# Performance work log

Hardware: AMD Instinct MI355X
Metric: run time of the kernel (lower is better)

## Reference

```python
import jax, jax.numpy as jnp
import numpy as np

EMBED_DIM = 1024
NUM_HEADS = 16
HEAD_DIM = EMBED_DIM // NUM_HEADS
SCALE = HEAD_DIM ** -0.5


def setup_inputs() -> dict:
    key = jax.random.key(0)
    k_x, k_wqkv, k_bqkv, k_wp, k_bp = jax.random.split(key, 5)
    B, N = 2, 2048
    x = jax.random.normal(k_x, (B, N, EMBED_DIM), dtype=jnp.float32)
    # torch.nn.Linear default init: U(-1/sqrt(fan_in), 1/sqrt(fan_in))
    lim = 1.0 / np.sqrt(EMBED_DIM)
    W_qkv = jax.random.uniform(k_wqkv, (EMBED_DIM, 3 * EMBED_DIM), jnp.float32, -lim, lim)
    b_qkv = jax.random.uniform(k_bqkv, (3 * EMBED_DIM,), jnp.float32, -lim, lim)
    W_proj = jax.random.uniform(k_wp, (EMBED_DIM, EMBED_DIM), jnp.float32, -lim, lim)
    b_proj = jax.random.uniform(k_bp, (EMBED_DIM,), jnp.float32, -lim, lim)
    return {"x": x, "W_qkv": W_qkv, "b_qkv": b_qkv, "W_proj": W_proj, "b_proj": b_proj}


def reference(x, W_qkv, b_qkv, W_proj, b_proj):
    B, N, C = x.shape
    qkv = x @ W_qkv + b_qkv                              # [B, N, 3C]
    qkv = qkv.reshape(B, N, 3, NUM_HEADS, HEAD_DIM)
    qkv = jnp.transpose(qkv, (2, 0, 3, 1, 4))            # [3, B, H, N, D]
    q, k, v = qkv[0], qkv[1], qkv[2]
    attn = jnp.einsum('bhnd,bhmd->bhnm', q, k) * SCALE   # [B, H, N, N]
    attn = jax.nn.softmax(attn, axis=-1)
    out = jnp.einsum('bhnm,bhmd->bhnd', attn, v)         # [B, H, N, D]
    out = jnp.transpose(out, (0, 2, 1, 3)).reshape(B, N, C)
    return out @ W_proj + b_proj
```

## Files before the change

kernel.cpp:

```cpp
#include <hip/hip_runtime.h>
#include <math.h>

typedef unsigned short u16;
typedef _Float16 f16;
typedef f16 f16x8 __attribute__((ext_vector_type(8)));
typedef __fp16 hp16x2 __attribute__((ext_vector_type(2)));
typedef float f32x4 __attribute__((ext_vector_type(4)));
typedef float f32x16 __attribute__((ext_vector_type(16)));

#define SEQ   2048
#define NH    16
#define HD    64
#define EMB   1024
#define NQKV  3072
#define BATCH 2
#define PSTR  72
#define QSCALE 0.18033688f

__device__ __forceinline__ u16 f2h(float f) {
  union { f16 h; u16 u; } w; w.h = (f16)f; return w.u;
}

__device__ __forceinline__ void gload16(const void* g, void* l) {
  __builtin_amdgcn_global_load_lds(
      (const __attribute__((address_space(1))) unsigned int*)g,
      (__attribute__((address_space(3))) unsigned int*)l, 16, 0, 0);
}

__global__ __launch_bounds__(256) void cvt_x(const float* __restrict__ X,
                                             u16* __restrict__ Xh) {
  const size_t i = ((size_t)blockIdx.x * 256 + threadIdx.x) * 8;
  float4 a = *reinterpret_cast<const float4*>(&X[i]);
  float4 b = *reinterpret_cast<const float4*>(&X[i + 4]);
  union { hp16x2 h2[4]; float4 f; } pk;
  pk.h2[0] = __builtin_amdgcn_cvt_pkrtz(a.x, a.y);
  pk.h2[1] = __builtin_amdgcn_cvt_pkrtz(a.z, a.w);
  pk.h2[2] = __builtin_amdgcn_cvt_pkrtz(b.x, b.y);
  pk.h2[3] = __builtin_amdgcn_cvt_pkrtz(b.z, b.w);
  *reinterpret_cast<float4*>(&Xh[i]) = pk.f;
}

__global__ __launch_bounds__(256) void cvt_wt(const float* __restrict__ W,
                                              u16* __restrict__ Wt,
                                              int K, int N) {
  __shared__ u16 T[64][68];
  const int n0 = blockIdx.x << 6, k0 = blockIdx.y << 6;
  const int t = threadIdx.x;
  const int rr = t >> 4, cc = (t & 15) << 2;
#pragma unroll
  for (int p = 0; p < 4; p++) {
    const int kr = p * 16 + rr;
    float4 v = *reinterpret_cast<const float4*>(&W[(size_t)(k0 + kr) * N + n0 + cc]);
    T[cc + 0][kr] = f2h(v.x); T[cc + 1][kr] = f2h(v.y);
    T[cc + 2][kr] = f2h(v.z); T[cc + 3][kr] = f2h(v.w);
  }
  __syncthreads();
#pragma unroll
  for (int p = 0; p < 4; p++) {
    const int nr = p * 16 + rr;
    union { u16 s[4]; unsigned long long d; } o;
    o.s[0] = T[nr][cc + 0]; o.s[1] = T[nr][cc + 1];
    o.s[2] = T[nr][cc + 2]; o.s[3] = T[nr][cc + 3];
    *reinterpret_cast<unsigned long long*>(&Wt[(size_t)(n0 + nr) * K + k0 + cc]) = o.d;
  }
}

__device__ __forceinline__ void gemm_core(const u16* __restrict__ Ag,
                                          const u16* __restrict__ Bg,
                                          int m0, int n0, int t,
                                          f32x4 acc[4][4]) {
  __shared__ __align__(16) u16 As[128 * 32];
  __shared__ __align__(16) u16 Bs[128 * 32];
  const int lane = t & 63, w = t >> 6;
  const int l15  = lane & 15, quad = lane >> 4;
  const int wm = w >> 1, wn = w & 1;
  const int srow  = lane >> 2;
  const int gslot = (lane & 3) ^ ((srow >> 1) & 3);
  const int xk    = (quad ^ ((l15 >> 1) & 3)) << 3;

  for (int k0 = 0; k0 < EMB; k0 += 32) {
    __syncthreads();
#pragma unroll
    for (int i = 0; i < 2; i++) {
      const int ca = w * 2 + i;
      const int arow = ca * 16 + srow;
      gload16(Ag + (size_t)(m0 + arow) * EMB + k0 + gslot * 8, &As[ca * 512]);
      gload16(Bg + (size_t)(n0 + arow) * EMB + k0 + gslot * 8, &Bs[ca * 512]);
    }
    __syncthreads();
    f16x8 af[4], bf[4];
#pragma unroll
    for (int s = 0; s < 4; s++)
      af[s] = *reinterpret_cast<const f16x8*>(&As[(wm * 64 + s * 16 + l15) * 32 + xk]);
#pragma unroll
    for (int s = 0; s < 4; s++)
      bf[s] = *reinterpret_cast<const f16x8*>(&Bs[(wn * 64 + s * 16 + l15) * 32 + xk]);
#pragma unroll
    for (int i = 0; i < 4; i++)
#pragma unroll
      for (int j = 0; j < 4; j++)
        acc[i][j] = __builtin_amdgcn_mfma_f32_16x16x32_f16(af[i], bf[j], acc[i][j], 0, 0, 0);
  }
}

__global__ __launch_bounds__(256) void k_qkv(const u16* __restrict__ Ag,
                                             const u16* __restrict__ Bg,
                                             const float* __restrict__ bias,
                                             u16* __restrict__ qo,
                                             u16* __restrict__ ko,
                                             u16* __restrict__ vo) {
  const int t = threadIdx.x;
  const int lane = t & 63, w = t >> 6;
  const int l15 = lane & 15, quad = lane >> 4;
  const int wm = w >> 1, wn = w & 1;
  const int m0 = blockIdx.y << 7, n0 = blockIdx.x << 7;
  f32x4 acc[4][4];
#pragma unroll
  for (int i = 0; i < 4; i++)
#pragma unroll
    for (int j = 0; j < 4; j++) acc[i][j] = (f32x4){0.f, 0.f, 0.f, 0.f};
  gemm_core(Ag, Bg, m0, n0, t, acc);
#pragma unroll
  for (int j = 0; j < 4; j++) {
    const int c = n0 + wn * 64 + j * 16 + l15;
    const int which = c >> 10, h = (c >> 6) & 15, d = c & 63;
    const float bv = bias[c];
    const float sc = (which == 0) ? QSCALE : 1.0f;
#pragma unroll
    for (int i = 0; i < 4; i++) {
#pragma unroll
      for (int r = 0; r < 4; r++) {
        const int m  = m0 + wm * 64 + i * 16 + quad * 4 + r;
        const int bb = m >> 11, n = m & (SEQ - 1);
        const u16 val = f2h((acc[i][j][r] + bv) * sc);
        if (which == 2)
          vo[(((size_t)bb * NH + h) * HD + d) * SEQ + n] = val;
        else if (which == 1)
          ko[((((size_t)bb * NH + h) * SEQ) + n) * HD + d] = val;
        else
          qo[((((size_t)bb * NH + h) * SEQ) + n) * HD + d] = val;
      }
    }
  }
}

__global__ __launch_bounds__(256) void k_proj(const u16* __restrict__ Ag,
                                              const u16* __restrict__ Bg,
                                              const float* __restrict__ bias,
                                              float* __restrict__ out) {
  const int t = threadIdx.x;
  const int lane = t & 63, w = t >> 6;
  const int l15 = lane & 15, quad = lane >> 4;
  const int wm = w >> 1, wn = w & 1;
  const int m0 = blockIdx.y << 7, n0 = blockIdx.x << 7;
  f32x4 acc[4][4];
#pragma unroll
  for (int i = 0; i < 4; i++)
#pragma unroll
    for (int j = 0; j < 4; j++) acc[i][j] = (f32x4){0.f, 0.f, 0.f, 0.f};
  gemm_core(Ag, Bg, m0, n0, t, acc);
#pragma unroll
  for (int j = 0; j < 4; j++) {
    const int c = n0 + wn * 64 + j * 16 + l15;
    const float bv = bias[c];
#pragma unroll
    for (int i = 0; i < 4; i++) {
#pragma unroll
      for (int r = 0; r < 4; r++) {
        const int m = m0 + wm * 64 + i * 16 + quad * 4 + r;
        out[(size_t)m * EMB + c] = acc[i][j][r] + bv;
      }
    }
  }
}

__global__ __launch_bounds__(256) void k_attn(const u16* __restrict__ Qg,
                                              const u16* __restrict__ Kg,
                                              const u16* __restrict__ Vtg,
                                              u16* __restrict__ AO) {
  __shared__ __align__(16) u16 Ks[64 * 64];
  __shared__ __align__(16) u16 Vs[64 * 64];
  __shared__ __align__(16) u16 Ps[4 * 32 * PSTR];
  const int t    = threadIdx.x;
  const int lane = t & 63, w = t >> 6;
  const int l31  = lane & 31, hi = lane >> 5;
  const int bh   = blockIdx.y;
  const int q0   = blockIdx.x << 7;
  const size_t base = (size_t)bh * SEQ * HD;

  f16x8 qf[4];
  {
    const u16* qp = Qg + base + (size_t)(q0 + 32 * w + l31) * HD + hi * 8;
#pragma unroll
    for (int c = 0; c < 4; c++) {
      union { float4 f; f16x8 v; } fu;
      fu.f = *reinterpret_cast<const float4*>(qp + c * 16);
      qf[c] = fu.v;
    }
  }

  f32x16 O0 = {}, O1 = {};
  float lsum = 0.f;
  const int fsw = (l31 >> 1) & 7;
  const int srw = lane >> 3, ssl = lane & 7;
  u16* Pw = &Ps[w * 32 * PSTR];

  for (int kt = 0; kt < SEQ; kt += 64) {
    __syncthreads();
#pragma unroll
    for (int i = 0; i < 2; i++) {
      const int ca  = w * 2 + i;
      const int row = ca * 8 + srw;
      const int sg  = (ssl ^ ((row >> 1) & 7)) << 3;
      gload16(Kg  + base + (size_t)(kt + row) * HD + sg, &Ks[ca * 512]);
      gload16(Vtg + base + (size_t)row * SEQ + kt + sg,  &Vs[ca * 512]);
    }
    __syncthreads();

#pragma unroll
    for (int sk = 0; sk < 2; sk++) {
      f32x16 c = {};
#pragma unroll
      for (int cc = 0; cc < 4; cc++) {
        f16x8 kf = *reinterpret_cast<const f16x8*>(
            &Ks[(sk * 32 + l31) * 64 + (((cc * 2 + hi) ^ fsw) << 3)]);
        c = __builtin_amdgcn_mfma_f32_32x32x16_f16(kf, qf[cc], c, 0, 0, 0);
      }
#pragma unroll
      for (int g = 0; g < 4; g++) {
        const float p0 = exp2f(c[4 * g + 0]);
        const float p1 = exp2f(c[4 * g + 1]);
        const float p2 = exp2f(c[4 * g + 2]);
        const float p3 = exp2f(c[4 * g + 3]);
        lsum += (p0 + p1) + (p2 + p3);
        union { hp16x2 h2[2]; unsigned long long d; } pk;
        pk.h2[0] = __builtin_amdgcn_cvt_pkrtz(p0, p1);
        pk.h2[1] = __builtin_amdgcn_cvt_pkrtz(p2, p3);
        *reinterpret_cast<unsigned long long*>(
            &Pw[l31 * PSTR + sk * 32 + g * 8 + 4 * hi]) = pk.d;
      }
    }

#pragma unroll
    for (int cc = 0; cc < 4; cc++) {
      f16x8 pf = *reinterpret_cast<const f16x8*>(&Pw[l31 * PSTR + cc * 16 + hi * 8]);
      f16x8 vf0 = *reinterpret_cast<const f16x8*>(
          &Vs[l31 * 64 + (((cc * 2 + hi) ^ fsw) << 3)]);
      f16x8 vf1 = *reinterpret_cast<const f16x8*>(
          &Vs[(32 + l31) * 64 + (((cc * 2 + hi) ^ fsw) << 3)]);
      O0 = __builtin_amdgcn_mfma_f32_32x32x16_f16(pf, vf0, O0, 0, 0, 0);
      O1 = __builtin_amdgcn_mfma_f32_32x32x16_f16(pf, vf1, O1, 0, 0, 0);
    }
  }

  lsum += __shfl_xor(lsum, 32);
  const int b = bh >> 4, h = bh & 15;
#pragma unroll
  for (int g = 0; g < 4; g++) {
#pragma unroll
    for (int rr = 0; rr < 4; rr++) {
      const int r = g * 4 + rr;
      const int qrow = rr + 8 * g + 4 * hi;
      const float inv = 1.f / __shfl(lsum, qrow, 64);
      const int n = q0 + 32 * w + qrow;
      u16* dst = AO + ((size_t)(b * SEQ + n)) * EMB + h * HD;
      dst[l31]      = f2h(O0[r] * inv);
      dst[32 + l31] = f2h(O1[r] * inv);
    }
  }
}

extern "C" void kernel_launch(void* const* d_in, const int* in_sizes, int n_in,
                              void* d_out, int out_size, void* d_ws, size_t ws_size,
                              hipStream_t stream) {
  (void)in_sizes; (void)n_in; (void)out_size; (void)ws_size;
  const float* x     = (const float*)d_in[0];
  const float* Wqkv  = (const float*)d_in[1];
  const float* bqkv  = (const float*)d_in[2];
  const float* Wproj = (const float*)d_in[3];
  const float* bproj = (const float*)d_in[4];
  float* out = (float*)d_out;

  const size_t NE = (size_t)BATCH * SEQ * EMB;
  u16* q    = (u16*)d_ws;
  u16* k    = q + NE;
  u16* vt   = k + NE;
  u16* aoxh = vt + NE;
  u16* Wt   = aoxh + NE;
  u16* Wpt  = Wt + (size_t)NQKV * EMB;

  cvt_x<<<NE / 2048, 256, 0, stream>>>(x, aoxh);
  dim3 gw1(NQKV / 64, EMB / 64);
  cvt_wt<<<gw1, 256, 0, stream>>>(Wqkv, Wt, EMB, NQKV);
  dim3 gw2(EMB / 64, EMB / 64);
  cvt_wt<<<gw2, 256, 0, stream>>>(Wproj, Wpt, EMB, EMB);

  dim3 gq(NQKV / 128, (BATCH * SEQ) / 128);
  k_qkv<<<gq, 256, 0, stream>>>(aoxh, Wt, bqkv, q, k, vt);

  dim3 ga(SEQ / 128, BATCH * NH);
  k_attn<<<ga, 256, 0, stream>>>(q, k, vt, aoxh);

  dim3 gp(EMB / 128, (BATCH * SEQ) / 128);
  k_proj<<<gp, 256, 0, stream>>>(aoxh, Wpt, bproj, out);
}
```

Measured before the change: 220.7 us.

## Split attention key range across two wave groups and pass P through registers

The attention block grows to 512 threads. Two groups of four waves each cover half of the key sequence for the same 128 query rows, then merge partial O and row sums through shared memory. The P tile no longer goes through an LDS staging buffer: packed fp16 probabilities are rearranged with cross-half shuffles into the MFMA operand layout. This aims to double parallelism per query tile, since the grid is only 512 blocks, and to cut LDS traffic, at the cost of a final reduction step and larger blocks.

```diff
diff --git a/kernel.cpp b/kernel.cpp
--- a/kernel.cpp
+++ b/kernel.cpp
@@ -14,7 +14,6 @@
 #define EMB   1024
 #define NQKV  3072
 #define BATCH 2
-#define PSTR  72
 #define QSCALE 0.18033688f
 
 __device__ __forceinline__ u16 f2h(float f) {
@@ -174,23 +173,26 @@
   }
 }
 
-__global__ __launch_bounds__(256) void k_attn(const u16* __restrict__ Qg,
-                                              const u16* __restrict__ Kg,
-                                              const u16* __restrict__ Vtg,
-                                              u16* __restrict__ AO) {
-  __shared__ __align__(16) u16 Ks[64 * 64];
-  __shared__ __align__(16) u16 Vs[64 * 64];
-  __shared__ __align__(16) u16 Ps[4 * 32 * PSTR];
+__global__ __launch_bounds__(512, 4) void k_attn(const u16* __restrict__ Qg,
+                                                 const u16* __restrict__ Kg,
+                                                 const u16* __restrict__ Vtg,
+                                                 u16* __restrict__ AO) {
+  __shared__ __align__(16) u16 KV[2][2][64 * 64];
+  __shared__ float Lx[256];
   const int t    = threadIdx.x;
   const int lane = t & 63, w = t >> 6;
+  const int grp  = w >> 2, wl = w & 3;
   const int l31  = lane & 31, hi = lane >> 5;
   const int bh   = blockIdx.y;
   const int q0   = blockIdx.x << 7;
   const size_t base = (size_t)bh * SEQ * HD;
 
+  u16* Ks = KV[grp][0];
+  u16* Vs = KV[grp][1];
+
   f16x8 qf[4];
   {
-    const u16* qp = Qg + base + (size_t)(q0 + 32 * w + l31) * HD + hi * 8;
+    const u16* qp = Qg + base + (size_t)(q0 + 32 * wl + l31) * HD + hi * 8;
 #pragma unroll
     for (int c = 0; c < 4; c++) {
       union { float4 f; f16x8 v; } fu;
@@ -203,13 +205,13 @@
   float lsum = 0.f;
   const int fsw = (l31 >> 1) & 7;
   const int srw = lane >> 3, ssl = lane & 7;
-  u16* Pw = &Ps[w * 32 * PSTR];
-
-  for (int kt = 0; kt < SEQ; kt += 64) {
+  const int kbeg = grp << 10;
+
+  for (int kt = kbeg; kt < kbeg + (SEQ / 2); kt += 64) {
     __syncthreads();
 #pragma unroll
     for (int i = 0; i < 2; i++) {
-      const int ca  = w * 2 + i;
+      const int ca  = wl * 2 + i;
       const int row = ca * 8 + srw;
       const int sg  = (ssl ^ ((row >> 1) & 7)) << 3;
       gload16(Kg  + base + (size_t)(kt + row) * HD + sg, &Ks[ca * 512]);
@@ -226,6 +228,7 @@
             &Ks[(sk * 32 + l31) * 64 + (((cc * 2 + hi) ^ fsw) << 3)]);
         c = __builtin_amdgcn_mfma_f32_32x32x16_f16(kf, qf[cc], c, 0, 0, 0);
       }
+      unsigned pw[4][2];
 #pragma unroll
       for (int g = 0; g < 4; g++) {
         const float p0 = exp2f(c[4 * g + 0]);
@@ -233,39 +236,73 @@
         const float p2 = exp2f(c[4 * g + 2]);
         const float p3 = exp2f(c[4 * g + 3]);
         lsum += (p0 + p1) + (p2 + p3);
-        union { hp16x2 h2[2]; unsigned long long d; } pk;
-        pk.h2[0] = __builtin_amdgcn_cvt_pkrtz(p0, p1);
-        pk.h2[1] = __builtin_amdgcn_cvt_pkrtz(p2, p3);
-        *reinterpret_cast<unsigned long long*>(
-            &Pw[l31 * PSTR + sk * 32 + g * 8 + 4 * hi]) = pk.d;
-      }
-    }
-
-#pragma unroll
-    for (int cc = 0; cc < 4; cc++) {
-      f16x8 pf = *reinterpret_cast<const f16x8*>(&Pw[l31 * PSTR + cc * 16 + hi * 8]);
-      f16x8 vf0 = *reinterpret_cast<const f16x8*>(
-          &Vs[l31 * 64 + (((cc * 2 + hi) ^ fsw) << 3)]);
-      f16x8 vf1 = *reinterpret_cast<const f16x8*>(
-          &Vs[(32 + l31) * 64 + (((cc * 2 + hi) ^ fsw) << 3)]);
-      O0 = __builtin_amdgcn_mfma_f32_32x32x16_f16(pf, vf0, O0, 0, 0, 0);
-      O1 = __builtin_amdgcn_mfma_f32_32x32x16_f16(pf, vf1, O1, 0, 0, 0);
-    }
-  }
-
-  lsum += __shfl_xor(lsum, 32);
-  const int b = bh >> 4, h = bh & 15;
-#pragma unroll
-  for (int g = 0; g < 4; g++) {
-#pragma unroll
-    for (int rr = 0; rr < 4; rr++) {
-      const int r = g * 4 + rr;
-      const int qrow = rr + 8 * g + 4 * hi;
-      const float inv = 1.f / __shfl(lsum, qrow, 64);
-      const int n = q0 + 32 * w + qrow;
-      u16* dst = AO + ((size_t)(b * SEQ + n)) * EMB + h * HD;
-      dst[l31]      = f2h(O0[r] * inv);
-      dst[32 + l31] = f2h(O1[r] * inv);
+        union { hp16x2 h; unsigned u; } w0, w1;
+        w0.h = __builtin_amdgcn_cvt_pkrtz(p0, p1);
+        w1.h = __builtin_amdgcn_cvt_pkrtz(p2, p3);
+        pw[g][0] = w0.u; pw[g][1] = w1.u;
+      }
+#pragma unroll
+      for (int s = 0; s < 2; s++) {
+        const unsigned a0 = pw[2 * s][0],     a1 = pw[2 * s][1];
+        const unsigned b0 = pw[2 * s + 1][0], b1 = pw[2 * s + 1][1];
+        const unsigned x0 = (unsigned)__shfl_xor((int)(hi ? a0 : b0), 32);
+        const unsigned x1 = (unsigned)__shfl_xor((int)(hi ? a1 : b1), 32);
+        union { unsigned u[4]; f16x8 v; } fr;
+        fr.u[0] = hi ? x0 : a0;
+        fr.u[1] = hi ? x1 : a1;
+        fr.u[2] = hi ? b0 : x0;
+        fr.u[3] = hi ? b1 : x1;
+        const int cc = sk * 2 + s;
+        f16x8 vf0 = *reinterpret_cast<const f16x8*>(
+            &Vs[l31 * 64 + (((cc * 2 + hi) ^ fsw) << 3)]);
+        f16x8 vf1 = *reinterpret_cast<const f16x8*>(
+            &Vs[(32 + l31) * 64 + (((cc * 2 + hi) ^ fsw) << 3)]);
+        O0 = __builtin_amdgcn_mfma_f32_32x32x16_f16(fr.v, vf0, O0, 0, 0, 0);
+        O1 = __builtin_amdgcn_mfma_f32_32x32x16_f16(fr.v, vf1, O1, 0, 0, 0);
+      }
+    }
+  }
+
+  __syncthreads();
+  float* Xch = reinterpret_cast<float*>(&KV[0][0][0]);
+  const int li = wl * 64 + lane;
+  if (grp == 1) {
+#pragma unroll
+    for (int g4 = 0; g4 < 4; g4++) {
+      f32x4 v0 = { O0[4 * g4 + 0], O0[4 * g4 + 1], O0[4 * g4 + 2], O0[4 * g4 + 3] };
+      *reinterpret_cast<f32x4*>(&Xch[(g4 * 256 + li) * 4]) = v0;
+      f32x4 v1 = { O1[4 * g4 + 0], O1[4 * g4 + 1], O1[4 * g4 + 2], O1[4 * g4 + 3] };
+      *reinterpret_cast<f32x4*>(&Xch[((4 + g4) * 256 + li) * 4]) = v1;
+    }
+    Lx[li] = lsum;
+  }
+  __syncthreads();
+  if (grp == 0) {
+#pragma unroll
+    for (int g4 = 0; g4 < 4; g4++) {
+      f32x4 v0 = *reinterpret_cast<const f32x4*>(&Xch[(g4 * 256 + li) * 4]);
+      f32x4 v1 = *reinterpret_cast<const f32x4*>(&Xch[((4 + g4) * 256 + li) * 4]);
+#pragma unroll
+      for (int j = 0; j < 4; j++) {
+        O0[4 * g4 + j] += v0[j];
+        O1[4 * g4 + j] += v1[j];
+      }
+    }
+    lsum += Lx[li];
+    lsum += __shfl_xor(lsum, 32);
+    const int b = bh >> 4, h = bh & 15;
+#pragma unroll
+    for (int g = 0; g < 4; g++) {
+#pragma unroll
+      for (int rr = 0; rr < 4; rr++) {
+        const int r = g * 4 + rr;
+        const int qrow = rr + 8 * g + 4 * hi;
+        const float inv = 1.f / __shfl(lsum, qrow, 64);
+        const int n = q0 + 32 * wl + qrow;
+        u16* dst = AO + ((size_t)(b * SEQ + n)) * EMB + h * HD;
+        dst[l31]      = f2h(O0[r] * inv);
+        dst[32 + l31] = f2h(O1[r] * inv);
+      }
     }
   }
 }
@@ -299,7 +336,7 @@
   k_qkv<<<gq, 256, 0, stream>>>(aoxh, Wt, bqkv, q, k, vt);
 
   dim3 ga(SEQ / 128, BATCH * NH);
-  k_attn<<<ga, 256, 0, stream>>>(q, k, vt, aoxh);
+  k_attn<<<ga, 512, 0, stream>>>(q, k, vt, aoxh);
 
   dim3 gp(EMB / 128, (BATCH * SEQ) / 128);
   k_proj<<<gp, 256, 0, stream>>>(aoxh, Wpt, bproj, out);
```

New measurement: 208.1 us. 1.06x faster.
